# Optimization experiments

Measured on AMD Instinct MI355X. Metric: run time of the kernel, lower is better.

Reference implementation:

```python
import jax, jax.numpy as jnp
import numpy as np

N_NODES = 50000
N_EDGES = 800000
IN_DIM = 128
HID_DIM = 64
N_HEADS = 4
OUT_DIM = 128
NEG_SLOPE = 0.2  # DGL GATConv default


def gat_conv(x, src, dst, W, attn_l, attn_r, bias, n_nodes):
    """DGL GATConv forward. x:[N,Fin], W:[Fin,H*D], attn_*:[H,D], bias:[H,D]. Returns [N,H,D]."""
    H, D = attn_l.shape
    h = (x @ W).reshape(n_nodes, H, D)              # [N,H,D]
    el = jnp.sum(h * attn_l[None], axis=-1)          # [N,H]
    er = jnp.sum(h * attn_r[None], axis=-1)          # [N,H]
    e = jax.nn.leaky_relu(el[src] + er[dst], NEG_SLOPE)  # [E,H]
    # edge softmax over incoming edges of each dst node (stable)
    m = jax.ops.segment_max(e, dst, num_segments=n_nodes)   # [N,H], -inf for empty
    ex = jnp.exp(e - m[dst])                                 # [E,H]
    denom = jax.ops.segment_sum(ex, dst, num_segments=n_nodes)  # [N,H]
    alpha = ex / denom[dst]                                  # [E,H]
    out = jax.ops.segment_sum(alpha[:, :, None] * h[src], dst, num_segments=n_nodes)
    return out + bias[None]                                  # [N,H,D]


def setup_inputs() -> dict:
    key = jax.random.key(0)
    ks = jax.random.split(key, 12)
    x = jax.random.normal(ks[0], (N_NODES, IN_DIM), dtype=jnp.float32)
    src = jax.random.randint(ks[1], (N_EDGES,), 0, N_NODES, dtype=jnp.int32)
    dst = jax.random.randint(ks[2], (N_EDGES,), 0, N_NODES, dtype=jnp.int32)
    s1 = 1.0 / np.sqrt(IN_DIM)
    s2 = 1.0 / np.sqrt(HID_DIM * N_HEADS)
    W1 = jax.random.normal(ks[3], (IN_DIM, N_HEADS * HID_DIM), dtype=jnp.float32) * s1
    al1 = jax.random.normal(ks[4], (N_HEADS, HID_DIM), dtype=jnp.float32) * 0.1
    ar1 = jax.random.normal(ks[5], (N_HEADS, HID_DIM), dtype=jnp.float32) * 0.1
    b1 = jnp.zeros((N_HEADS, HID_DIM), dtype=jnp.float32)
    W2 = jax.random.normal(ks[6], (N_HEADS * HID_DIM, OUT_DIM), dtype=jnp.float32) * s2
    al2 = jax.random.normal(ks[7], (1, OUT_DIM), dtype=jnp.float32) * 0.1
    ar2 = jax.random.normal(ks[8], (1, OUT_DIM), dtype=jnp.float32) * 0.1
    b2 = jnp.zeros((1, OUT_DIM), dtype=jnp.float32)
    return {"x": x, "src": src, "dst": dst, "W1": W1, "al1": al1, "ar1": ar1,
            "b1": b1, "W2": W2, "al2": al2, "ar2": ar2, "b2": b2}


def reference(x, src, dst, W1, al1, ar1, b1, W2, al2, ar2, b2):
    n = x.shape[0]
    h1 = gat_conv(x, src, dst, W1, al1, ar1, b1, n)          # [N,H,D]
    h1 = jax.nn.relu(h1).reshape(n, -1)                       # [N,H*D]
    h2 = gat_conv(h1, src, dst, W2, al2, ar2, b2, n)          # [N,1,OUT]
    return h2.reshape(n, -1)                                   # [N,OUT]
```

## Files before the change

### kernel.cpp

```cpp
#include <hip/hip_runtime.h>
#include <hip/hip_bf16.h>
#include <math.h>


#define NEG_SLOPE 0.2f
#define NB 256
#define CH 8192

typedef short short8 __attribute__((ext_vector_type(8)));
typedef float float4v __attribute__((ext_vector_type(4)));
typedef float float2v __attribute__((ext_vector_type(2)));

static __device__ __forceinline__ float lrelu(float v) {
    return v > 0.f ? v : NEG_SLOPE * v;
}

static __device__ __forceinline__ unsigned short f2bf(float f) {
    unsigned int u = __float_as_uint(f);
    u = (u + 0x7fffu + ((u >> 16) & 1u)) >> 16;
    return (unsigned short)u;
}
static __device__ __forceinline__ float bf2f(unsigned int lo16) {
    return __uint_as_float(lo16 << 16);
}

static __device__ __forceinline__ int bucket_of(int d, unsigned int M) {
    return (int)(((unsigned long long)(unsigned int)d * M) >> 32);
}

static __device__ __forceinline__ void pk_step(float2v& a00, float2v& a01,
                                               float2v& a10, float2v& a11,
                                               float2v& d0, float2v& d1,
                                               float4 w, unsigned int v) {
    float2v w01; w01[0] = w.x; w01[1] = w.y;
    float2v w23; w23[0] = w.z; w23[1] = w.w;
    float x0 = __uint_as_float(v << 16);
    float x1 = __uint_as_float(v & 0xffff0000u);
    float2v xx0 = {x0, x0};
    float2v xx1 = {x1, x1};
    asm("v_pk_fma_f32 %0, %1, %2, %0" : "+v"(a00) : "v"(w01), "v"(xx0));
    asm("v_pk_fma_f32 %0, %1, %2, %0" : "+v"(a01) : "v"(w23), "v"(xx0));
    asm("v_pk_fma_f32 %0, %1, %2, %0" : "+v"(a10) : "v"(w01), "v"(xx1));
    asm("v_pk_fma_f32 %0, %1, %2, %0" : "+v"(a11) : "v"(w23), "v"(xx1));
    asm("v_pk_add_f32 %0, %1, %0" : "+v"(d0) : "v"(w01));
    asm("v_pk_add_f32 %0, %1, %0" : "+v"(d1) : "v"(w23));
}


__global__ __launch_bounds__(256) void histbin_kernel(
        const int* __restrict__ dst, int* __restrict__ bcnt,
        int E, unsigned int M, int nblk,
        const float* __restrict__ W1, const float* __restrict__ al1,
        const float* __restrict__ ar1, const float* __restrict__ W2,
        const float* __restrict__ al2, const float* __restrict__ ar2,
        unsigned short* __restrict__ W1th, unsigned short* __restrict__ Qt1,
        unsigned short* __restrict__ Qt2, unsigned short* __restrict__ W2t) {
    int b = blockIdx.x;
    int tid = threadIdx.x;
    if (b < nblk) {
        __shared__ int lcnt[NB];
        lcnt[tid] = 0;
        __syncthreads();
        int e0 = b * CH;
        for (int i = tid; i < CH; i += 256) {
            int e = e0 + i;
            if (e < E) atomicAdd(&lcnt[bucket_of(dst[e], M)], 1);
        }
        __syncthreads();
        bcnt[b * NB + tid] = lcnt[tid];
        return;
    }
    int idx = (b - nblk) * 256 + tid;
    if (idx < 32768) {
        int h = idx >> 13;
        int r = idx & 8191;
        int d = r >> 7, k = r & 127;
        W1th[idx] = f2bf(W1[k * 256 + h * 64 + d]);
    } else if (idx < 34816) {
        int j = idx - 32768;
        int c = j >> 7, k = j & 127;
        float s = 0.f;
        if (c < 8) {
            int h = c & 3;
            const float* av = ((c < 4) ? al1 : ar1) + h * 64;
            const float* wrow = W1 + k * 256 + h * 64;
            #pragma unroll 8
            for (int d = 0; d < 64; ++d) s += wrow[d] * av[d];
        }
        Qt1[j] = f2bf(s);
    } else if (idx < 36864) {
        int j = idx - 34816;
        int c = j >> 7, k = j & 127;
        float s = (c == 0) ? al2[k] : (c == 1) ? ar2[k] : 0.f;
        Qt2[j] = f2bf(s);
    } else if (idx < 69632) {
        int j = idx - 36864;
        int m = j >> 8, k = j & 255;
        W2t[(size_t)m * 256 + k] = f2bf(W2[(size_t)k * 128 + m]);
    }
}


__global__ __launch_bounds__(256) void binscan_kernel(
        const int* __restrict__ bcnt, int* __restrict__ base,
        int* __restrict__ bucketStart, int nblk, int E) {
    __shared__ int s[NB];
    int t = threadIdx.x;
    int run = 0;
    for (int blk = 0; blk < nblk; ++blk) {
        int c = bcnt[blk * NB + t];
        base[blk * NB + t] = run;
        run += c;
    }
    int tot = run;
    s[t] = tot;
    __syncthreads();
    for (int off = 1; off < NB; off <<= 1) {
        int add = (t >= off) ? s[t - off] : 0;
        __syncthreads();
        s[t] += add;
        __syncthreads();
    }
    bucketStart[t] = s[t] - tot;
    if (t == NB - 1) bucketStart[NB] = E;
}


__global__ __launch_bounds__(256) void binscatter_kernel(
        const int* __restrict__ src, const int* __restrict__ dst,
        const int* __restrict__ base, const int* __restrict__ bucketStart,
        uint2* __restrict__ pairs, int E, unsigned int M) {
    __shared__ int cur[NB];
    int b = blockIdx.x;
    int tid = threadIdx.x;
    cur[tid] = base[b * NB + tid] + bucketStart[tid];
    __syncthreads();
    int e0 = b * CH;
    for (int i = tid; i < CH; i += 256) {
        int e = e0 + i;
        if (e < E) {
            int d = dst[e];
            int bk = bucket_of(d, M);
            int pos = atomicAdd(&cur[bk], 1);
            pairs[pos] = make_uint2((unsigned int)src[e], (unsigned int)d);
        }
    }
}


__global__ __launch_bounds__(256) void bucketcsr_kernel(
        const uint2* __restrict__ pairs, const int* __restrict__ bucketStart,
        int* __restrict__ row_start, int* __restrict__ srcs,
        int N, int npb, int E) {
    __shared__ int cnt[NB];
    __shared__ int sc[NB];
    int b = blockIdx.x;
    int tid = threadIdx.x;
    int nb0 = b * npb;
    int es = bucketStart[b], ee = bucketStart[b + 1];
    cnt[tid] = 0;
    __syncthreads();
    for (int i = es + tid; i < ee; i += 256) {
        uint2 p = pairs[i];
        atomicAdd(&cnt[(int)p.y - nb0], 1);
    }
    __syncthreads();
    int myc = cnt[tid];
    sc[tid] = myc;
    __syncthreads();
    for (int off = 1; off < NB; off <<= 1) {
        int add = (tid >= off) ? sc[tid - off] : 0;
        __syncthreads();
        sc[tid] += add;
        __syncthreads();
    }
    int excl = sc[tid] - myc;
    int n = nb0 + tid;
    if (n < N && tid < npb) row_start[n] = es + excl;
    if (b == gridDim.x - 1 && tid == 0) row_start[N] = E;
    cnt[tid] = es + excl;
    __syncthreads();
    for (int i = es + tid; i < ee; i += 256) {
        uint2 p = pairs[i];
        int pos = atomicAdd(&cnt[(int)p.y - nb0], 1);
        srcs[pos] = (int)p.x;
    }
}


__global__ __launch_bounds__(256) void xdots_kernel(
        const float* __restrict__ x, const unsigned short* __restrict__ Qt,
        unsigned short* __restrict__ xb,
        float* __restrict__ el, float* __restrict__ er, int N) {
    constexpr int KP = 136;
    __shared__ unsigned short As[64 * KP];
    __shared__ unsigned short Bs[16 * KP];
    const int tid = threadIdx.x;
    const int wid = tid >> 6, lane = tid & 63;
    const int r0 = blockIdx.x * 64;
    for (int ch = tid; ch < 64 * 16; ch += 256) {
        int row = ch >> 4, kc = ch & 15;
        int gr = r0 + row;
        short8 v = {};
        if (gr < N) {
            float4 a = *(const float4*)(x + (size_t)gr * 128 + kc * 8);
            float4 b = *(const float4*)(x + (size_t)gr * 128 + kc * 8 + 4);
            v[0] = (short)f2bf(a.x); v[1] = (short)f2bf(a.y);
            v[2] = (short)f2bf(a.z); v[3] = (short)f2bf(a.w);
            v[4] = (short)f2bf(b.x); v[5] = (short)f2bf(b.y);
            v[6] = (short)f2bf(b.z); v[7] = (short)f2bf(b.w);
            *(short8*)(xb + (size_t)gr * 128 + kc * 8) = v;
        }
        *(short8*)(As + row * KP + kc * 8) = v;
    }
    {
        int row = tid >> 4, kc = tid & 15;
        *(short8*)(Bs + row * KP + kc * 8) = *(const short8*)(Qt + row * 128 + kc * 8);
    }
    __syncthreads();
    float4v acc = (float4v){0.f, 0.f, 0.f, 0.f};
    const int lr = lane & 15, lk = (lane >> 4) * 8;
    #pragma unroll
    for (int ks = 0; ks < 128; ks += 32) {
        short8 af = *(const short8*)(As + (wid * 16 + lr) * KP + ks + lk);
        short8 bf_ = *(const short8*)(Bs + lr * KP + ks + lk);
        acc = __builtin_amdgcn_mfma_f32_16x16x32_bf16(af, bf_, acc, 0, 0, 0);
    }
    const int rbase = r0 + wid * 16 + (lane >> 4) * 4;
    #pragma unroll
    for (int j = 0; j < 4; ++j) {
        int row = rbase + j;
        if (row < N) {
            if (lr < 4) el[(size_t)row * 4 + lr] = acc[j];
            else if (lr < 8) er[(size_t)row * 4 + (lr - 4)] = acc[j];
        }
    }
}


__global__ __launch_bounds__(256) void dots2_kernel(
        const unsigned short* __restrict__ hb, const unsigned short* __restrict__ Qt,
        float* __restrict__ el, float* __restrict__ er, int N) {
    constexpr int KP = 136;
    __shared__ unsigned short As[64 * KP];
    __shared__ unsigned short Bs[16 * KP];
    const int tid = threadIdx.x;
    const int wid = tid >> 6, lane = tid & 63;
    const int r0 = blockIdx.x * 64;
    for (int ch = tid; ch < 64 * 16; ch += 256) {
        int row = ch >> 4, kc = ch & 15;
        int gr = r0 + row;
        short8 v = {};
        if (gr < N) v = *(const short8*)(hb + (size_t)gr * 128 + kc * 8);
        *(short8*)(As + row * KP + kc * 8) = v;
    }
    {
        int row = tid >> 4, kc = tid & 15;
        *(short8*)(Bs + row * KP + kc * 8) = *(const short8*)(Qt + row * 128 + kc * 8);
    }
    __syncthreads();
    float4v acc = (float4v){0.f, 0.f, 0.f, 0.f};
    const int lr = lane & 15, lk = (lane >> 4) * 8;
    #pragma unroll
    for (int ks = 0; ks < 128; ks += 32) {
        short8 af = *(const short8*)(As + (wid * 16 + lr) * KP + ks + lk);
        short8 bf_ = *(const short8*)(Bs + lr * KP + ks + lk);
        acc = __builtin_amdgcn_mfma_f32_16x16x32_bf16(af, bf_, acc, 0, 0, 0);
    }
    const int rbase = r0 + wid * 16 + (lane >> 4) * 4;
    #pragma unroll
    for (int j = 0; j < 4; ++j) {
        int row = rbase + j;
        if (row < N) {
            if (lr == 0) el[row] = acc[j];
            else if (lr == 1) er[row] = acc[j];
        }
    }
}


__global__ __launch_bounds__(256) void agg1x_kernel(const unsigned short* __restrict__ xb,
                            const float* __restrict__ el, const float* __restrict__ er,
                            const int* __restrict__ srcs, const int* __restrict__ row_start,
                            unsigned short* __restrict__ A1, int N) {
    __shared__ int   s_tbl[4][64];
    __shared__ float a_tbl[4][64][4];
    const int wslot = threadIdx.x >> 6;
    const int lane = threadIdx.x & 63;
    const int n = (blockIdx.x * 256 + threadIdx.x) >> 6;
    if (n >= N) return;
    const int rs = row_start[n];
    const int re = row_start[n + 1];

    float2v accP[2][2];
    accP[0][0] = (float2v){0.f, 0.f}; accP[0][1] = (float2v){0.f, 0.f};
    accP[1][0] = (float2v){0.f, 0.f}; accP[1][1] = (float2v){0.f, 0.f};
    float2v dP[2];
    dP[0] = (float2v){0.f, 0.f}; dP[1] = (float2v){0.f, 0.f};

    if (re > rs) {
        const float4 ern = *(const float4*)(er + (size_t)n * 4);
        for (int base = rs; base < re; base += 64) {
            const int cnt = (re - base) < 64 ? (re - base) : 64;
            asm volatile("s_waitcnt lgkmcnt(0)" ::: "memory");
            if (lane < cnt) {
                int sv = srcs[base + lane];
                float4 ev = *(const float4*)(el + (size_t)sv * 4);
                float4 av;
                av.x = __expf(lrelu(ev.x + ern.x));
                av.y = __expf(lrelu(ev.y + ern.y));
                av.z = __expf(lrelu(ev.z + ern.z));
                av.w = __expf(lrelu(ev.w + ern.w));
                s_tbl[wslot][lane] = sv;
                *(float4*)&a_tbl[wslot][lane][0] = av;
            }
            asm volatile("s_waitcnt lgkmcnt(0)" ::: "memory");
            int i = 0;
            for (; i + 4 <= cnt; i += 4) {
                int s0 = s_tbl[wslot][i],     s1 = s_tbl[wslot][i + 1];
                int s2 = s_tbl[wslot][i + 2], s3 = s_tbl[wslot][i + 3];
                float4 w0 = *(const float4*)&a_tbl[wslot][i][0];
                float4 w1 = *(const float4*)&a_tbl[wslot][i + 1][0];
                float4 w2 = *(const float4*)&a_tbl[wslot][i + 2][0];
                float4 w3 = *(const float4*)&a_tbl[wslot][i + 3][0];
                unsigned int v0 = *(const unsigned int*)(xb + (size_t)s0 * 128 + lane * 2);
                unsigned int v1 = *(const unsigned int*)(xb + (size_t)s1 * 128 + lane * 2);
                unsigned int v2 = *(const unsigned int*)(xb + (size_t)s2 * 128 + lane * 2);
                unsigned int v3 = *(const unsigned int*)(xb + (size_t)s3 * 128 + lane * 2);
                pk_step(accP[0][0], accP[0][1], accP[1][0], accP[1][1], dP[0], dP[1], w0, v0);
                pk_step(accP[0][0], accP[0][1], accP[1][0], accP[1][1], dP[0], dP[1], w1, v1);
                pk_step(accP[0][0], accP[0][1], accP[1][0], accP[1][1], dP[0], dP[1], w2, v2);
                pk_step(accP[0][0], accP[0][1], accP[1][0], accP[1][1], dP[0], dP[1], w3, v3);
            }
            for (; i < cnt; ++i) {
                int s0 = s_tbl[wslot][i];
                float4 w = *(const float4*)&a_tbl[wslot][i][0];
                unsigned int v = *(const unsigned int*)(xb + (size_t)s0 * 128 + lane * 2);
                pk_step(accP[0][0], accP[0][1], accP[1][0], accP[1][1], dP[0], dP[1], w, v);
            }
        }
        float i0 = 1.f / dP[0][0], i1 = 1.f / dP[0][1];
        float i2 = 1.f / dP[1][0], i3 = 1.f / dP[1][1];
        accP[0][0][0] *= i0; accP[1][0][0] *= i0;
        accP[0][0][1] *= i1; accP[1][0][1] *= i1;
        accP[0][1][0] *= i2; accP[1][1][0] *= i2;
        accP[0][1][1] *= i3; accP[1][1][1] *= i3;
    }
    unsigned int pk;
    pk = (unsigned int)f2bf(accP[0][0][0]) | ((unsigned int)f2bf(accP[1][0][0]) << 16);
    *(unsigned int*)(A1 + (size_t)n * 512 + 0 * 128 + lane * 2) = pk;
    pk = (unsigned int)f2bf(accP[0][0][1]) | ((unsigned int)f2bf(accP[1][0][1]) << 16);
    *(unsigned int*)(A1 + (size_t)n * 512 + 1 * 128 + lane * 2) = pk;
    pk = (unsigned int)f2bf(accP[0][1][0]) | ((unsigned int)f2bf(accP[1][1][0]) << 16);
    *(unsigned int*)(A1 + (size_t)n * 512 + 2 * 128 + lane * 2) = pk;
    pk = (unsigned int)f2bf(accP[0][1][1]) | ((unsigned int)f2bf(accP[1][1][1]) << 16);
    *(unsigned int*)(A1 + (size_t)n * 512 + 3 * 128 + lane * 2) = pk;
}


__global__ __launch_bounds__(256) void gemm1h_kernel(
        const unsigned short* __restrict__ A1,
        const unsigned short* __restrict__ W1th,
        const float* __restrict__ b1,
        unsigned short* __restrict__ h1rb,
        int N) {
    constexpr int KP = 136;
    __shared__ unsigned short As[128 * KP];
    __shared__ unsigned short Bs[64 * KP];
    const int tid = threadIdx.x;
    const int wid = tid >> 6;
    const int lane = tid & 63;
    const int r0 = blockIdx.x * 128;
    const int h = blockIdx.z;

    for (int ch = tid; ch < 128 * 16; ch += 256) {
        int row = ch >> 4, kc = ch & 15;
        int gr = r0 + row;
        short8 v = {};
        if (gr < N) v = *(const short8*)(A1 + (size_t)gr * 512 + h * 128 + kc * 8);
        *(short8*)(As + row * KP + kc * 8) = v;
    }
    for (int ch = tid; ch < 64 * 16; ch += 256) {
        int row = ch >> 4, kc = ch & 15;
        *(short8*)(Bs + row * KP + kc * 8) =
            *(const short8*)(W1th + (size_t)h * 8192 + row * 128 + kc * 8);
    }
    __syncthreads();

    float4v acc[8];
    #pragma unroll
    for (int fr = 0; fr < 8; ++fr) acc[fr] = (float4v){0.f, 0.f, 0.f, 0.f};

    const int lr = lane & 15;
    const int lk = (lane >> 4) * 8;
    const int cw = wid * 16;

    #pragma unroll
    for (int ks = 0; ks < 128; ks += 32) {
        short8 bfr = *(const short8*)(Bs + (cw + lr) * KP + ks + lk);
        #pragma unroll
        for (int fr = 0; fr < 8; ++fr) {
            short8 af = *(const short8*)(As + (fr * 16 + lr) * KP + ks + lk);
            acc[fr] = __builtin_amdgcn_mfma_f32_16x16x32_bf16(af, bfr, acc[fr], 0, 0, 0);
        }
    }

    const int col = h * 64 + cw + lr;
    const float bias = b1[col];
    const int rbase = r0 + (lane >> 4) * 4;
    #pragma unroll
    for (int fr = 0; fr < 8; ++fr) {
        #pragma unroll
        for (int j = 0; j < 4; ++j) {
            int row = rbase + fr * 16 + j;
            if (row < N)
                h1rb[(size_t)row * 256 + col] = f2bf(fmaxf(acc[fr][j] + bias, 0.f));
        }
    }
}


template <int K, int MSLICE>
__global__ __launch_bounds__(256) void mfma_gemm_kernel(
        const unsigned short* __restrict__ A,
        const unsigned short* __restrict__ Bt,
        unsigned short* __restrict__ C,
        int N, int Mtot) {
    constexpr int KP = K + 8;
    constexpr int CF = MSLICE / 64;
    constexpr int KC = K / 8;
    __shared__ unsigned short As[64 * KP];
    __shared__ unsigned short Bs[MSLICE * KP];
    const int tid = threadIdx.x;
    const int wid = tid >> 6;
    const int lane = tid & 63;
    const int r0 = blockIdx.x * 64;
    const int c0 = blockIdx.y * MSLICE;

    for (int ch = tid; ch < 64 * KC; ch += 256) {
        int row = ch / KC, kc = ch - row * KC;
        int gr = r0 + row;
        short8 v = {};
        if (gr < N) v = *(const short8*)(A + (size_t)gr * K + kc * 8);
        *(short8*)(As + row * KP + kc * 8) = v;
    }
    for (int ch = tid; ch < MSLICE * KC; ch += 256) {
        int row = ch / KC, kc = ch - row * KC;
        *(short8*)(Bs + row * KP + kc * 8) =
            *(const short8*)(Bt + (size_t)(c0 + row) * K + kc * 8);
    }
    __syncthreads();

    float4v acc[4][CF];
    #pragma unroll
    for (int fr = 0; fr < 4; ++fr)
        #pragma unroll
        for (int cf = 0; cf < CF; ++cf)
            acc[fr][cf] = (float4v){0.f, 0.f, 0.f, 0.f};

    const int lr = lane & 15;
    const int lk = (lane >> 4) * 8;
    const int cw = wid * (MSLICE / 4);

    #pragma unroll
    for (int ks = 0; ks < K; ks += 32) {
        short8 af[4], bfr[CF];
        #pragma unroll
        for (int fr = 0; fr < 4; ++fr)
            af[fr] = *(const short8*)(As + (fr * 16 + lr) * KP + ks + lk);
        #pragma unroll
        for (int cf = 0; cf < CF; ++cf)
            bfr[cf] = *(const short8*)(Bs + (cw + cf * 16 + lr) * KP + ks + lk);
        #pragma unroll
        for (int fr = 0; fr < 4; ++fr)
            #pragma unroll
            for (int cf = 0; cf < CF; ++cf)
                acc[fr][cf] = __builtin_amdgcn_mfma_f32_16x16x32_bf16(
                    af[fr], bfr[cf], acc[fr][cf], 0, 0, 0);
    }

    const int rbase = r0 + (lane >> 4) * 4;
    #pragma unroll
    for (int fr = 0; fr < 4; ++fr) {
        #pragma unroll
        for (int cf = 0; cf < CF; ++cf) {
            int col = c0 + cw + cf * 16 + lr;
            #pragma unroll
            for (int j = 0; j < 4; ++j) {
                int row = rbase + fr * 16 + j;
                if (row < N)
                    C[(size_t)row * Mtot + col] = f2bf(acc[fr][cf][j]);
            }
        }
    }
}


__global__ __launch_bounds__(256) void agg2_kernel(const unsigned short* __restrict__ hb,
                           const float* __restrict__ el, const float* __restrict__ er,
                           const int* __restrict__ srcs, const int* __restrict__ row_start,
                           const float* __restrict__ bias, float* __restrict__ out, int N) {
    __shared__ uint2 t_tbl[4][64];
    const int wslot = threadIdx.x >> 6;
    const int lane = threadIdx.x & 63;
    const int n = (blockIdx.x * 256 + threadIdx.x) >> 6;
    if (n >= N) return;
    const int rs = row_start[n];
    const int re = row_start[n + 1];

    float acc0 = 0.f, acc1 = 0.f, d = 0.f;

    if (re > rs) {
        const float ern = er[n];
        for (int base = rs; base < re; base += 64) {
            const int cnt = (re - base) < 64 ? (re - base) : 64;
            asm volatile("s_waitcnt lgkmcnt(0)" ::: "memory");
            if (lane < cnt) {
                int sv = srcs[base + lane];
                float a = __expf(lrelu(el[sv] + ern));
                t_tbl[wslot][lane] = make_uint2((unsigned int)sv, __float_as_uint(a));
            }
            asm volatile("s_waitcnt lgkmcnt(0)" ::: "memory");
            int i = 0;
            for (; i + 4 <= cnt; i += 4) {
                uint2 t0 = t_tbl[wslot][i],     t1 = t_tbl[wslot][i + 1];
                uint2 t2 = t_tbl[wslot][i + 2], t3 = t_tbl[wslot][i + 3];
                float w0 = __uint_as_float(t0.y), w1 = __uint_as_float(t1.y);
                float w2 = __uint_as_float(t2.y), w3 = __uint_as_float(t3.y);
                unsigned int v0 = *(const unsigned int*)(hb + (size_t)t0.x * 128 + lane * 2);
                unsigned int v1 = *(const unsigned int*)(hb + (size_t)t1.x * 128 + lane * 2);
                unsigned int v2 = *(const unsigned int*)(hb + (size_t)t2.x * 128 + lane * 2);
                unsigned int v3 = *(const unsigned int*)(hb + (size_t)t3.x * 128 + lane * 2);
                d += w0 + w1 + w2 + w3;
                acc0 += w0 * bf2f(v0 & 0xffffu) + w1 * bf2f(v1 & 0xffffu) +
                        w2 * bf2f(v2 & 0xffffu) + w3 * bf2f(v3 & 0xffffu);
                acc1 += w0 * bf2f(v0 >> 16) + w1 * bf2f(v1 >> 16) +
                        w2 * bf2f(v2 >> 16) + w3 * bf2f(v3 >> 16);
            }
            for (; i < cnt; ++i) {
                uint2 t = t_tbl[wslot][i];
                float w = __uint_as_float(t.y);
                unsigned int v = *(const unsigned int*)(hb + (size_t)t.x * 128 + lane * 2);
                d += w;
                acc0 += w * bf2f(v & 0xffffu);
                acc1 += w * bf2f(v >> 16);
            }
        }
        float invd = 1.f / d;
        acc0 *= invd; acc1 *= invd;
    }
    float o0 = acc0 + bias[lane * 2];
    float o1 = acc1 + bias[lane * 2 + 1];
    *(float2*)(out + (size_t)n * 128 + lane * 2) = make_float2(o0, o1);
}


extern "C" void kernel_launch(void* const* d_in, const int* in_sizes, int n_in,
                              void* d_out, int out_size, void* d_ws, size_t ws_size,
                              hipStream_t stream) {
    const float* x   = (const float*)d_in[0];
    const int*   src = (const int*)d_in[1];
    const int*   dst = (const int*)d_in[2];
    const float* W1  = (const float*)d_in[3];
    const float* al1 = (const float*)d_in[4];
    const float* ar1 = (const float*)d_in[5];
    const float* b1  = (const float*)d_in[6];
    const float* W2  = (const float*)d_in[7];
    const float* al2 = (const float*)d_in[8];
    const float* ar2 = (const float*)d_in[9];
    const float* b2  = (const float*)d_in[10];
    float* out = (float*)d_out;

    const int N = in_sizes[0] / 128;
    const int E = in_sizes[1];
    const int npb = (N + NB - 1) / NB;
    const unsigned int M =
        (unsigned int)(((1ULL << 32) + npb - 1) / (unsigned long long)npb);
    const int nblk_e = (E + CH - 1) / CH;

    char* ws = (char*)d_ws;
    size_t oXB   = 0;
    size_t oA1   = oXB + (size_t)N * 128 * 2;
    size_t oH1R  = oA1 + (size_t)N * 512 * 2;
    size_t oW1th = oH1R + (size_t)N * 256 * 2;
    size_t oQt1  = oW1th + 32768 * 2;
    size_t oQt2  = oQt1 + 2048 * 2;
    size_t oW2t  = oQt2 + 2048 * 2;
    size_t oEl1  = oW2t + 32768 * 2;
    size_t oEr1  = oEl1 + (size_t)N * 4 * 4;
    size_t oEl2  = oEr1 + (size_t)N * 4 * 4;
    size_t oEr2  = oEl2 + (size_t)N * 4;
    size_t oRow  = oEr2 + (size_t)N * 4;
    size_t oBcnt = oRow + (((size_t)(N + 1) * 4 + 15) & ~(size_t)15);
    size_t oBase = oBcnt + (size_t)nblk_e * NB * 4;
    size_t oBkS  = oBase + (size_t)nblk_e * NB * 4;
    size_t oPair = (oBkS + (NB + 1) * 4 + 15) & ~(size_t)15;
    size_t oSrcs = oPair + (size_t)E * 8;

    unsigned short* xb   = (unsigned short*)(ws + oXB);
    unsigned short* A1   = (unsigned short*)(ws + oA1);
    unsigned short* h2b  = (unsigned short*)(ws + oA1);
    unsigned short* h1rb = (unsigned short*)(ws + oH1R);
    unsigned short* w1th = (unsigned short*)(ws + oW1th);
    unsigned short* qt1  = (unsigned short*)(ws + oQt1);
    unsigned short* qt2  = (unsigned short*)(ws + oQt2);
    unsigned short* w2t  = (unsigned short*)(ws + oW2t);
    float* el1 = (float*)(ws + oEl1);
    float* er1 = (float*)(ws + oEr1);
    float* el2 = (float*)(ws + oEl2);
    float* er2 = (float*)(ws + oEr2);
    int*   row_start   = (int*)(ws + oRow);
    int*   bcnt        = (int*)(ws + oBcnt);
    int*   base        = (int*)(ws + oBase);
    int*   bucketStart = (int*)(ws + oBkS);
    uint2* pairs       = (uint2*)(ws + oPair);
    int*   srcs        = (int*)(ws + oSrcs);

    histbin_kernel<<<nblk_e + 272, 256, 0, stream>>>(
        dst, bcnt, E, M, nblk_e, W1, al1, ar1, W2, al2, ar2, w1th, qt1, qt2, w2t);
    binscan_kernel<<<1, 256, 0, stream>>>(bcnt, base, bucketStart, nblk_e, E);
    binscatter_kernel<<<nblk_e, 256, 0, stream>>>(src, dst, base, bucketStart, pairs, E, M);
    bucketcsr_kernel<<<NB, 256, 0, stream>>>(pairs, bucketStart, row_start, srcs, N, npb, E);

    const int nrowb = (N + 63) / 64;
    const int nrowb2 = (N + 127) / 128;
    const int nwaveb = (N + 3) / 4;

    xdots_kernel<<<nrowb, 256, 0, stream>>>(x, qt1, xb, el1, er1, N);
    agg1x_kernel<<<nwaveb, 256, 0, stream>>>(xb, el1, er1, srcs, row_start, A1, N);
    gemm1h_kernel<<<dim3(nrowb2, 1, 4), 256, 0, stream>>>(A1, w1th, b1, h1rb, N);

    mfma_gemm_kernel<256, 64><<<dim3(nrowb, 2), 256, 0, stream>>>(h1rb, w2t, h2b, N, 128);
    dots2_kernel<<<nrowb, 256, 0, stream>>>(h2b, qt2, el2, er2, N);
    agg2_kernel<<<nwaveb, 256, 0, stream>>>(h2b, el2, er2, srcs, row_start, b2, out, N);
}
```

Baseline: 209.3 us.

## Fuse bin scan into scatter and co-launch scatter with xdots blocks

Drops the single-block binscan kernel. Each scatter block now recomputes its own prefix base and the bucket starts redundantly from the per-block histogram counts. The scatter blocks are merged into one launch with the independent xdots GEMM blocks, which share a union shared-memory buffer. This removes two kernel launches and the serial single-block scan, so scatter work can overlap the feature projection. In exchange, every scatter block now repeats the scan over nblk rows of counts.

```diff
diff --git a/kernel.cpp b/kernel.cpp
--- a/kernel.cpp
+++ b/kernel.cpp
@@ -101,103 +101,58 @@
 }
 
 
-__global__ __launch_bounds__(256) void binscan_kernel(
-        const int* __restrict__ bcnt, int* __restrict__ base,
-        int* __restrict__ bucketStart, int nblk, int E) {
-    __shared__ int s[NB];
-    int t = threadIdx.x;
-    int run = 0;
-    for (int blk = 0; blk < nblk; ++blk) {
-        int c = bcnt[blk * NB + t];
-        base[blk * NB + t] = run;
-        run += c;
-    }
-    int tot = run;
-    s[t] = tot;
-    __syncthreads();
-    for (int off = 1; off < NB; off <<= 1) {
-        int add = (t >= off) ? s[t - off] : 0;
-        __syncthreads();
-        s[t] += add;
-        __syncthreads();
-    }
-    bucketStart[t] = s[t] - tot;
-    if (t == NB - 1) bucketStart[NB] = E;
-}
-
-
-__global__ __launch_bounds__(256) void binscatter_kernel(
+__global__ __launch_bounds__(256) void scatxdots_kernel(
         const int* __restrict__ src, const int* __restrict__ dst,
-        const int* __restrict__ base, const int* __restrict__ bucketStart,
-        uint2* __restrict__ pairs, int E, unsigned int M) {
-    __shared__ int cur[NB];
-    int b = blockIdx.x;
-    int tid = threadIdx.x;
-    cur[tid] = base[b * NB + tid] + bucketStart[tid];
-    __syncthreads();
-    int e0 = b * CH;
-    for (int i = tid; i < CH; i += 256) {
-        int e = e0 + i;
-        if (e < E) {
-            int d = dst[e];
-            int bk = bucket_of(d, M);
-            int pos = atomicAdd(&cur[bk], 1);
-            pairs[pos] = make_uint2((unsigned int)src[e], (unsigned int)d);
-        }
-    }
-}
-
-
-__global__ __launch_bounds__(256) void bucketcsr_kernel(
-        const uint2* __restrict__ pairs, const int* __restrict__ bucketStart,
-        int* __restrict__ row_start, int* __restrict__ srcs,
-        int N, int npb, int E) {
-    __shared__ int cnt[NB];
-    __shared__ int sc[NB];
-    int b = blockIdx.x;
-    int tid = threadIdx.x;
-    int nb0 = b * npb;
-    int es = bucketStart[b], ee = bucketStart[b + 1];
-    cnt[tid] = 0;
-    __syncthreads();
-    for (int i = es + tid; i < ee; i += 256) {
-        uint2 p = pairs[i];
-        atomicAdd(&cnt[(int)p.y - nb0], 1);
-    }
-    __syncthreads();
-    int myc = cnt[tid];
-    sc[tid] = myc;
-    __syncthreads();
-    for (int off = 1; off < NB; off <<= 1) {
-        int add = (tid >= off) ? sc[tid - off] : 0;
-        __syncthreads();
-        sc[tid] += add;
-        __syncthreads();
-    }
-    int excl = sc[tid] - myc;
-    int n = nb0 + tid;
-    if (n < N && tid < npb) row_start[n] = es + excl;
-    if (b == gridDim.x - 1 && tid == 0) row_start[N] = E;
-    cnt[tid] = es + excl;
-    __syncthreads();
-    for (int i = es + tid; i < ee; i += 256) {
-        uint2 p = pairs[i];
-        int pos = atomicAdd(&cnt[(int)p.y - nb0], 1);
-        srcs[pos] = (int)p.x;
-    }
-}
-
-
-__global__ __launch_bounds__(256) void xdots_kernel(
+        const int* __restrict__ bcnt, int* __restrict__ bucketStart,
+        uint2* __restrict__ pairs, int E, unsigned int M, int nblk,
         const float* __restrict__ x, const unsigned short* __restrict__ Qt,
         unsigned short* __restrict__ xb,
         float* __restrict__ el, float* __restrict__ er, int N) {
     constexpr int KP = 136;
-    __shared__ unsigned short As[64 * KP];
-    __shared__ unsigned short Bs[16 * KP];
+    __shared__ alignas(16) unsigned char smem[(64 + 16) * KP * 2];
     const int tid = threadIdx.x;
+    if (blockIdx.x < (unsigned)nblk) {
+        int* cur  = (int*)smem;
+        int* stmp = cur + NB;
+        const int b = blockIdx.x;
+        int run = 0, mybase = 0;
+        for (int blk = 0; blk < nblk; ++blk) {
+            int c = bcnt[blk * NB + tid];
+            if (blk == b) mybase = run;
+            run += c;
+        }
+        const int tot = run;
+        stmp[tid] = tot;
+        __syncthreads();
+        for (int off = 1; off < NB; off <<= 1) {
+            int add = (tid >= off) ? stmp[tid - off] : 0;
+            __syncthreads();
+            stmp[tid] += add;
+            __syncthreads();
+        }
+        const int bs = stmp[tid] - tot;
+        if (b == 0) {
+            bucketStart[tid] = bs;
+            if (tid == NB - 1) bucketStart[NB] = E;
+        }
+        cur[tid] = bs + mybase;
+        __syncthreads();
+        int e0 = b * CH;
+        for (int i = tid; i < CH; i += 256) {
+            int e = e0 + i;
+            if (e < E) {
+                int d = dst[e];
+                int bk = bucket_of(d, M);
+                int pos = atomicAdd(&cur[bk], 1);
+                pairs[pos] = make_uint2((unsigned int)src[e], (unsigned int)d);
+            }
+        }
+        return;
+    }
+    unsigned short* As = (unsigned short*)smem;
+    unsigned short* Bs = As + 64 * KP;
     const int wid = tid >> 6, lane = tid & 63;
-    const int r0 = blockIdx.x * 64;
+    const int r0 = (blockIdx.x - nblk) * 64;
     for (int ch = tid; ch < 64 * 16; ch += 256) {
         int row = ch >> 4, kc = ch & 15;
         int gr = r0 + row;
@@ -234,6 +189,46 @@
             if (lr < 4) el[(size_t)row * 4 + lr] = acc[j];
             else if (lr < 8) er[(size_t)row * 4 + (lr - 4)] = acc[j];
         }
+    }
+}
+
+
+__global__ __launch_bounds__(256) void bucketcsr_kernel(
+        const uint2* __restrict__ pairs, const int* __restrict__ bucketStart,
+        int* __restrict__ row_start, int* __restrict__ srcs,
+        int N, int npb, int E) {
+    __shared__ int cnt[NB];
+    __shared__ int sc[NB];
+    int b = blockIdx.x;
+    int tid = threadIdx.x;
+    int nb0 = b * npb;
+    int es = bucketStart[b], ee = bucketStart[b + 1];
+    cnt[tid] = 0;
+    __syncthreads();
+    for (int i = es + tid; i < ee; i += 256) {
+        uint2 p = pairs[i];
+        atomicAdd(&cnt[(int)p.y - nb0], 1);
+    }
+    __syncthreads();
+    int myc = cnt[tid];
+    sc[tid] = myc;
+    __syncthreads();
+    for (int off = 1; off < NB; off <<= 1) {
+        int add = (tid >= off) ? sc[tid - off] : 0;
+        __syncthreads();
+        sc[tid] += add;
+        __syncthreads();
+    }
+    int excl = sc[tid] - myc;
+    int n = nb0 + tid;
+    if (n < N && tid < npb) row_start[n] = es + excl;
+    if (b == gridDim.x - 1 && tid == 0) row_start[N] = E;
+    cnt[tid] = es + excl;
+    __syncthreads();
+    for (int i = es + tid; i < ee; i += 256) {
+        uint2 p = pairs[i];
+        int pos = atomicAdd(&cnt[(int)p.y - nb0], 1);
+        srcs[pos] = (int)p.x;
     }
 }
 
@@ -592,8 +587,7 @@
     size_t oEr2  = oEl2 + (size_t)N * 4;
     size_t oRow  = oEr2 + (size_t)N * 4;
     size_t oBcnt = oRow + (((size_t)(N + 1) * 4 + 15) & ~(size_t)15);
-    size_t oBase = oBcnt + (size_t)nblk_e * NB * 4;
-    size_t oBkS  = oBase + (size_t)nblk_e * NB * 4;
+    size_t oBkS  = oBcnt + (size_t)nblk_e * NB * 4;
     size_t oPair = (oBkS + (NB + 1) * 4 + 15) & ~(size_t)15;
     size_t oSrcs = oPair + (size_t)E * 8;
 
@@ -611,22 +605,23 @@
     float* er2 = (float*)(ws + oEr2);
     int*   row_start   = (int*)(ws + oRow);
     int*   bcnt        = (int*)(ws + oBcnt);
-    int*   base        = (int*)(ws + oBase);
     int*   bucketStart = (int*)(ws + oBkS);
     uint2* pairs       = (uint2*)(ws + oPair);
     int*   srcs        = (int*)(ws + oSrcs);
 
-    histbin_kernel<<<nblk_e + 272, 256, 0, stream>>>(
-        dst, bcnt, E, M, nblk_e, W1, al1, ar1, W2, al2, ar2, w1th, qt1, qt2, w2t);
-    binscan_kernel<<<1, 256, 0, stream>>>(bcnt, base, bucketStart, nblk_e, E);
-    binscatter_kernel<<<nblk_e, 256, 0, stream>>>(src, dst, base, bucketStart, pairs, E, M);
-    bucketcsr_kernel<<<NB, 256, 0, stream>>>(pairs, bucketStart, row_start, srcs, N, npb, E);
-
     const int nrowb = (N + 63) / 64;
     const int nrowb2 = (N + 127) / 128;
     const int nwaveb = (N + 3) / 4;
 
-    xdots_kernel<<<nrowb, 256, 0, stream>>>(x, qt1, xb, el1, er1, N);
+    histbin_kernel<<<nblk_e + 272, 256, 0, stream>>>(
+        dst, bcnt, E, M, nblk_e, W1, al1, ar1, W2, al2, ar2, w1th, qt1, qt2, w2t);
+
+    scatxdots_kernel<<<nblk_e + nrowb, 256, 0, stream>>>(
+        src, dst, bcnt, bucketStart, pairs, E, M, nblk_e,
+        x, qt1, xb, el1, er1, N);
+
+    bucketcsr_kernel<<<NB, 256, 0, stream>>>(pairs, bucketStart, row_start, srcs, N, npb, E);
+
     agg1x_kernel<<<nwaveb, 256, 0, stream>>>(xb, el1, er1, srcs, row_start, A1, N);
     gemm1h_kernel<<<dim3(nrowb2, 1, 4), 256, 0, stream>>>(A1, w1th, b1, h1rb, N);
 
```

Measured after the change: 204.0 us. 1.03x faster.
